# Kernel tuning notes

Hardware: AMD Instinct MI355X
Metric: run time of the kernel (lower is better)

The kernel has to match this reference:

```python
import jax, jax.numpy as jnp
import numpy as np

PH = 32          # prediction horizon (unroll steps)
HID = 512        # hidden_dim == latent_dim (output fed back as input)
OUT = 2          # output_dim
BS = 2048


def setup_inputs() -> dict:
    key = jax.random.key(0)
    ks = jax.random.split(key, 8)
    s = 1.0 / np.sqrt(HID)
    return {
        "hist": jax.random.normal(ks[0], (BS, 8, 2), dtype=jnp.float32),
        "z": jax.random.normal(ks[1], (BS, 1, HID), dtype=jnp.float32),
        # LSTMCell params (PyTorch layout: [4H, in], gate order i,f,g,o)
        "W_ih": jax.random.uniform(ks[2], (4 * HID, HID), jnp.float32, -s, s),
        "W_hh": jax.random.uniform(ks[3], (4 * HID, HID), jnp.float32, -s, s),
        "b_ih": jax.random.uniform(ks[4], (4 * HID,), jnp.float32, -s, s),
        "b_hh": jax.random.uniform(ks[5], (4 * HID,), jnp.float32, -s, s),
        # dense: hidden_dim -> output_dim
        "W_d": jax.random.uniform(ks[6], (OUT, HID), jnp.float32, -s, s),
        "b_d": jax.random.uniform(ks[7], (OUT,), jnp.float32, -s, s),
    }


def reference(hist, z, W_ih, W_hh, b_ih, b_hh, W_d, b_d):
    bs = z.shape[0]
    x0 = z.reshape(bs, -1)                       # [bs, H]
    h0 = jnp.zeros((bs, HID), dtype=z.dtype)
    c0 = jnp.zeros((bs, HID), dtype=z.dtype)

    def step(carry, _):
        x, h, c = carry
        gates = x @ W_ih.T + b_ih + h @ W_hh.T + b_hh   # [bs, 4H]
        i, f, g, o = jnp.split(gates, 4, axis=-1)
        c_new = jax.nn.sigmoid(f) * c + jax.nn.sigmoid(i) * jnp.tanh(g)
        h_new = jax.nn.sigmoid(o) * jnp.tanh(c_new)
        # output h is fed back as next input
        return (h_new, h_new, c_new), h_new

    _, hs = jax.lax.scan(step, (x0, h0, c0), None, length=PH)  # [PH, bs, H]
    out_all = jnp.swapaxes(hs, 0, 1)                           # [bs, PH, H]
    y = out_all @ W_d.T + b_d                                  # [bs, PH, OUT]
    return y
```

## Files before the change

kernel.cpp:

```cpp
#include <hip/hip_runtime.h>
#include <hip/hip_bf16.h>

#define BS_   2048
#define HID_  512
#define PH_   32

#define HWREG_XCC_ID ((3 << 11) | (0 << 6) | 20)

typedef _Float16 half8 __attribute__((ext_vector_type(8)));
typedef float floatx4 __attribute__((ext_vector_type(4)));

__device__ __forceinline__ float sigf(float x) { return 1.f / (1.f + __expf(-x)); }
__device__ __forceinline__ float tanhfast(float x) {
    float e = __expf(2.f * x);
    return 1.f - 2.f / (e + 1.f);
}

__global__ __launch_bounds__(256) void prep_kernel(
    const float* __restrict__ Wih, const float* __restrict__ Whh,
    const float* __restrict__ bih, const float* __restrict__ bhh,
    const float* __restrict__ z,
    _Float16* __restrict__ wih16, _Float16* __restrict__ wsum16,
    _Float16* __restrict__ z16, float* __restrict__ bsum,
    int* __restrict__ cnt)
{
    int i = blockIdx.x * 256 + threadIdx.x;
    if (i < BS_ * HID_) z16[i] = (_Float16)z[i];
    if (i < 4 * HID_ * HID_) {
        float a = Wih[i];
        wih16[i]  = (_Float16)a;
        wsum16[i] = (_Float16)(a + Whh[i]);
    }
    if (i < 4 * HID_) bsum[i] = bih[i] + bhh[i];
    if (i < 264) cnt[i] = 0;
}

__device__ __forceinline__ void stage_weights(_Float16* Wl, const _Float16* Wg,
                                              int j, int tid)
{
#pragma unroll
    for (int rep = 0; rep < 8; ++rep) {
        int idx = rep * 512 + tid;
        int n  = idx >> 6;
        int kb = idx & 63;
        int g  = n >> 4, u = n & 15;
        const half8* src = (const half8*)(Wg + ((size_t)(g * HID_ + j * 16 + u)) * HID_ + kb * 8);
        int phys = (kb & 56) | ((kb & 7) ^ (n & 7));
        *(half8*)((char*)Wl + n * 1024 + phys * 16) = *src;
    }
}

__global__ __launch_bounds__(512, 2) void lstm_persist(
    const _Float16* __restrict__ wih16, const _Float16* __restrict__ wsum16,
    const float* __restrict__ bsum, const _Float16* __restrict__ z16,
    _Float16* __restrict__ hs, int* __restrict__ cnt)
{
    __shared__ _Float16 Wl[64 * 512];

    const int tid  = threadIdx.x;
    const int ib   = blockIdx.x & 7;
    const int j    = blockIdx.x >> 3;
    const int lane = tid & 63;
    const int wv   = tid >> 6;
    const int qw   = lane >> 4;
    const int ln   = lane & 15;
    const int hid  = j * 16 + ln;

    stage_weights(Wl, wih16, j, tid);

    float bias[4];
#pragma unroll
    for (int g = 0; g < 4; ++g) bias[g] = bsum[g * HID_ + hid];

    float c[2][4];
#pragma unroll
    for (int mt = 0; mt < 2; ++mt)
#pragma unroll
        for (int r = 0; r < 4; ++r) c[mt][r] = 0.f;

    const char* Bl = (const char*)Wl;
    const int tE = (qw ^ (ln & 7)) * 16;

    bool fast = false;

    __syncthreads();

    for (int t = 0; t < PH_; ++t) {
        const _Float16* x = (t == 0) ? z16 : hs + (size_t)(t - 1) * BS_ * HID_;

        if (t >= 1) {
            if (tid == 0) {
                while (__hip_atomic_fetch_add(&cnt[ib * 32 + t - 1], 0,
                                              __ATOMIC_RELAXED,
                                              __HIP_MEMORY_SCOPE_AGENT) < 32) {
                    __builtin_amdgcn_s_sleep(1);
                }
                if (t == 1) {
                    __builtin_amdgcn_fence(__ATOMIC_ACQUIRE, "agent");
                    int m = __hip_atomic_fetch_add(&cnt[256 + ib], 0,
                                                   __ATOMIC_RELAXED,
                                                   __HIP_MEMORY_SCOPE_AGENT);
                    fast = (__popc((unsigned)m) == 1);
                } else if (fast) {
                    __builtin_amdgcn_fence(__ATOMIC_ACQUIRE, "workgroup");
                } else {
                    __builtin_amdgcn_fence(__ATOMIC_ACQUIRE, "agent");
                }
            }
            __syncthreads();
        }

        floatx4 acc[2][4];
#pragma unroll
        for (int mt = 0; mt < 2; ++mt)
#pragma unroll
            for (int g = 0; g < 4; ++g) acc[mt][g] = (floatx4){0.f, 0.f, 0.f, 0.f};

        const _Float16* A0 = x + (size_t)(ib * 256 + wv * 32 + ln) * HID_ + qw * 8;

#pragma unroll
        for (int kk = 0; kk < 16; ++kk) {
            half8 a0 = *(const half8*)(A0 + kk * 32);
            half8 a1 = *(const half8*)(A0 + 16 * HID_ + kk * 32);
            half8 b[4];
#pragma unroll
            for (int g = 0; g < 4; ++g) {
                int off = (g * 16 + ln) * 1024 + (kk >> 1) * 128 + (tE ^ ((kk & 1) << 6));
                b[g] = *(const half8*)(Bl + off);
            }
#pragma unroll
            for (int g = 0; g < 4; ++g) {
                acc[0][g] = __builtin_amdgcn_mfma_f32_16x16x32_f16(a0, b[g], acc[0][g], 0, 0, 0);
                acc[1][g] = __builtin_amdgcn_mfma_f32_16x16x32_f16(a1, b[g], acc[1][g], 0, 0, 0);
            }
        }

        _Float16* hb = hs + (size_t)t * BS_ * HID_
                          + (size_t)(ib * 256 + wv * 32 + qw * 4) * HID_ + hid;
#pragma unroll
        for (int mt = 0; mt < 2; ++mt) {
#pragma unroll
            for (int r = 0; r < 4; ++r) {
                float gi = acc[mt][0][r] + bias[0];
                float gf = acc[mt][1][r] + bias[1];
                float gg = acc[mt][2][r] + bias[2];
                float go = acc[mt][3][r] + bias[3];
                float cn = sigf(gf) * c[mt][r] + sigf(gi) * tanhfast(gg);
                float hn = sigf(go) * tanhfast(cn);
                c[mt][r] = cn;
                hb[(size_t)(mt * 16 + r) * HID_] = (_Float16)hn;
            }
        }

        __syncthreads();
        if (t == 0) {
            if (tid == 0) {
                int xcd = __builtin_amdgcn_s_getreg(HWREG_XCC_ID) & 0xf;
                __hip_atomic_fetch_or(&cnt[256 + ib], 1 << xcd,
                                      __ATOMIC_RELAXED, __HIP_MEMORY_SCOPE_AGENT);
                __threadfence();
                atomicAdd(&cnt[ib * 32 + 0], 1);
            }
            stage_weights(Wl, wsum16, j, tid);
            __syncthreads();
        } else if (t < PH_ - 1) {
            if (tid == 0) {
                if (fast) {
                    __hip_atomic_fetch_add(&cnt[ib * 32 + t], 1,
                                           __ATOMIC_RELAXED,
                                           __HIP_MEMORY_SCOPE_AGENT);
                } else {
                    __threadfence();
                    atomicAdd(&cnt[ib * 32 + t], 1);
                }
            }
        }
    }
}

__global__ __launch_bounds__(256) void dense_kernel(
    const _Float16* __restrict__ hs, const float* __restrict__ Wd,
    const float* __restrict__ bd, float* __restrict__ y)
{
    int gw   = (blockIdx.x * 256 + threadIdx.x) >> 6;
    int lane = threadIdx.x & 63;
    int tt = gw & 31, b = gw >> 5;
    half8 h = *(const half8*)(hs + ((size_t)tt * BS_ + b) * HID_ + lane * 8);
    float s0 = 0.f, s1 = 0.f;
#pragma unroll
    for (int k = 0; k < 8; ++k) {
        float hv = (float)h[k];
        s0 += hv * Wd[lane * 8 + k];
        s1 += hv * Wd[HID_ + lane * 8 + k];
    }
#pragma unroll
    for (int m = 32; m >= 1; m >>= 1) {
        s0 += __shfl_xor(s0, m);
        s1 += __shfl_xor(s1, m);
    }
    if (lane == 0) {
        float* o = y + ((size_t)b * PH_ + tt) * 2;
        o[0] = s0 + bd[0];
        o[1] = s1 + bd[1];
    }
}

extern "C" void kernel_launch(void* const* d_in, const int* in_sizes, int n_in,
                              void* d_out, int out_size, void* d_ws, size_t ws_size,
                              hipStream_t stream)
{
    (void)in_sizes; (void)n_in; (void)out_size; (void)ws_size;
    const float* z   = (const float*)d_in[1];
    const float* Wih = (const float*)d_in[2];
    const float* Whh = (const float*)d_in[3];
    const float* bih = (const float*)d_in[4];
    const float* bhh = (const float*)d_in[5];
    const float* Wd  = (const float*)d_in[6];
    const float* bd  = (const float*)d_in[7];
    float* y = (float*)d_out;

    char* ws = (char*)d_ws;
    _Float16* hs     = (_Float16*)ws;
    _Float16* z16    = (_Float16*)(ws + (size_t)67108864);
    _Float16* wih16  = (_Float16*)(ws + (size_t)69206016);
    _Float16* wsum16 = (_Float16*)(ws + (size_t)71303168);
    float*    bsum   = (float*)   (ws + (size_t)73400320);
    int*      cnt    = (int*)     (ws + (size_t)73408512);

    prep_kernel<<<4096, 256, 0, stream>>>(Wih, Whh, bih, bhh, z,
                                          wih16, wsum16, z16, bsum, cnt);

    {
        const void* k = (const void*)lstm_persist;
        void* args[] = {(void*)&wih16, (void*)&wsum16, (void*)&bsum,
                        (void*)&z16, (void*)&hs, (void*)&cnt};
        hipLaunchCooperativeKernel(k, dim3(256), dim3(512), args, 0, stream);
    }

    dense_kernel<<<16384, 256, 0, stream>>>(hs, Wd, bd, y);
}
```

Before: 474.1 us.

## Assign LSTM work tiles by XCD at runtime and software-pipeline MFMA operand loads

Each workgroup reads its XCC id and claims a slot so that all 32 column-blocks of one batch group land on the same XCD. Leftover workgroups take unclaimed slots after two grid barriers. This lets more groups use the cheaper workgroup-scope fence path for per-step synchronisation instead of agent-scope fences. The inner GEMM loop now prefetches A fragments four steps ahead and double-buffers the LDS B fragments, and the bias is folded into the accumulator initialisation. The cost is two extra grid barriers at startup and higher register pressure.

```diff
diff --git a/kernel.cpp b/kernel.cpp
--- a/kernel.cpp
+++ b/kernel.cpp
@@ -6,6 +6,14 @@
 #define PH_   32
 
 #define HWREG_XCC_ID ((3 << 11) | (0 << 6) | 20)
+
+#define C_STEP  0
+#define C_MASK  256
+#define C_SLOT  264
+#define C_SPILL 272
+#define C_GSYNC 288
+#define C_TAKEN 320
+#define C_TOTAL 576
 
 typedef _Float16 half8 __attribute__((ext_vector_type(8)));
 typedef float floatx4 __attribute__((ext_vector_type(4)));
@@ -32,7 +40,21 @@
         wsum16[i] = (_Float16)(a + Whh[i]);
     }
     if (i < 4 * HID_) bsum[i] = bih[i] + bhh[i];
-    if (i < 264) cnt[i] = 0;
+    if (i < C_TOTAL) cnt[i] = 0;
+}
+
+__device__ __forceinline__ void grid_sync(int* gc, int tid) {
+    __syncthreads();
+    if (tid == 0) {
+        __threadfence();
+        atomicAdd(gc, 1);
+        while (__hip_atomic_fetch_add(gc, 0, __ATOMIC_RELAXED,
+                                      __HIP_MEMORY_SCOPE_AGENT) < 256) {
+            __builtin_amdgcn_s_sleep(1);
+        }
+        __builtin_amdgcn_fence(__ATOMIC_ACQUIRE, "agent");
+    }
+    __syncthreads();
 }
 
 __device__ __forceinline__ void stage_weights(_Float16* Wl, const _Float16* Wg,
@@ -56,14 +78,53 @@
     _Float16* __restrict__ hs, int* __restrict__ cnt)
 {
     __shared__ _Float16 Wl[64 * 512];
+    __shared__ int sh_ctrl;
 
     const int tid  = threadIdx.x;
-    const int ib   = blockIdx.x & 7;
-    const int j    = blockIdx.x >> 3;
     const int lane = tid & 63;
     const int wv   = tid >> 6;
     const int qw   = lane >> 4;
     const int ln   = lane & 15;
+
+    int x = 0, mine = -1, rank = -1;
+    if (tid == 0) {
+        x = __builtin_amdgcn_s_getreg(HWREG_XCC_ID) & 7;
+        int s = __hip_atomic_fetch_add(&cnt[C_SLOT + x], 1, __ATOMIC_RELAXED,
+                                       __HIP_MEMORY_SCOPE_AGENT);
+        if (s < 32) {
+            mine = x * 32 + s;
+            cnt[C_TAKEN + mine] = 1;
+            __hip_atomic_fetch_or(&cnt[C_MASK + x], 1 << x, __ATOMIC_RELAXED,
+                                  __HIP_MEMORY_SCOPE_AGENT);
+        } else {
+            rank = __hip_atomic_fetch_add(&cnt[C_SPILL], 1, __ATOMIC_RELAXED,
+                                          __HIP_MEMORY_SCOPE_AGENT);
+        }
+    }
+    grid_sync(&cnt[C_GSYNC + 0], tid);
+    if (tid == 0 && mine < 0) {
+        int seen = 0;
+        for (int s = 0; s < 256; ++s) {
+            if (cnt[C_TAKEN + s] == 0) {
+                if (seen == rank) { mine = s; break; }
+                ++seen;
+            }
+        }
+        __hip_atomic_fetch_or(&cnt[C_MASK + (mine >> 5)], 1 << x,
+                              __ATOMIC_RELAXED, __HIP_MEMORY_SCOPE_AGENT);
+    }
+    grid_sync(&cnt[C_GSYNC + 1], tid);
+    if (tid == 0) {
+        int m = __hip_atomic_fetch_add(&cnt[C_MASK + (mine >> 5)], 0,
+                                       __ATOMIC_RELAXED, __HIP_MEMORY_SCOPE_AGENT);
+        int fastf = (__popc((unsigned)m) == 1) ? 1 : 0;
+        sh_ctrl = mine | (fastf << 16);
+    }
+    __syncthreads();
+    const int ctrl = sh_ctrl;
+    const int ib   = (ctrl & 0xffff) >> 5;
+    const int j    = ctrl & 31;
+    const bool fast = (ctrl >> 16) != 0;
     const int hid  = j * 16 + ln;
 
     stage_weights(Wl, wih16, j, tid);
@@ -81,57 +142,64 @@
     const char* Bl = (const char*)Wl;
     const int tE = (qw ^ (ln & 7)) * 16;
 
-    bool fast = false;
-
     __syncthreads();
 
     for (int t = 0; t < PH_; ++t) {
-        const _Float16* x = (t == 0) ? z16 : hs + (size_t)(t - 1) * BS_ * HID_;
+        const _Float16* xx = (t == 0) ? z16 : hs + (size_t)(t - 1) * BS_ * HID_;
 
         if (t >= 1) {
             if (tid == 0) {
-                while (__hip_atomic_fetch_add(&cnt[ib * 32 + t - 1], 0,
+                while (__hip_atomic_fetch_add(&cnt[C_STEP + ib * 32 + t - 1], 0,
                                               __ATOMIC_RELAXED,
                                               __HIP_MEMORY_SCOPE_AGENT) < 32) {
                     __builtin_amdgcn_s_sleep(1);
                 }
-                if (t == 1) {
-                    __builtin_amdgcn_fence(__ATOMIC_ACQUIRE, "agent");
-                    int m = __hip_atomic_fetch_add(&cnt[256 + ib], 0,
-                                                   __ATOMIC_RELAXED,
-                                                   __HIP_MEMORY_SCOPE_AGENT);
-                    fast = (__popc((unsigned)m) == 1);
-                } else if (fast) {
-                    __builtin_amdgcn_fence(__ATOMIC_ACQUIRE, "workgroup");
-                } else {
-                    __builtin_amdgcn_fence(__ATOMIC_ACQUIRE, "agent");
+                if (fast) __builtin_amdgcn_fence(__ATOMIC_ACQUIRE, "workgroup");
+                else      __builtin_amdgcn_fence(__ATOMIC_ACQUIRE, "agent");
+            }
+            __syncthreads();
+        }
+
+        floatx4 acc[2][4];
+#pragma unroll
+        for (int mt = 0; mt < 2; ++mt)
+#pragma unroll
+            for (int g = 0; g < 4; ++g)
+                acc[mt][g] = (floatx4){bias[g], bias[g], bias[g], bias[g]};
+
+        const _Float16* A0 = xx + (size_t)(ib * 256 + wv * 32 + ln) * HID_ + qw * 8;
+
+        half8 a0r[4], a1r[4], bA[4], bB[4];
+#pragma unroll
+        for (int p = 0; p < 4; ++p) {
+            a0r[p] = *(const half8*)(A0 + p * 32);
+            a1r[p] = *(const half8*)(A0 + 16 * HID_ + p * 32);
+        }
+#pragma unroll
+        for (int g = 0; g < 4; ++g)
+            bA[g] = *(const half8*)(Bl + (g * 16 + ln) * 1024 + tE);
+
+#pragma unroll
+        for (int kk = 0; kk < 16; ++kk) {
+            half8 ca0 = a0r[kk & 3], ca1 = a1r[kk & 3];
+            if (kk < 12) {
+                a0r[kk & 3] = *(const half8*)(A0 + (kk + 4) * 32);
+                a1r[kk & 3] = *(const half8*)(A0 + 16 * HID_ + (kk + 4) * 32);
+            }
+            half8* cb = (kk & 1) ? bB : bA;
+            half8* nb = (kk & 1) ? bA : bB;
+            if (kk < 15) {
+                int k1 = kk + 1;
+#pragma unroll
+                for (int g = 0; g < 4; ++g) {
+                    int off = (g * 16 + ln) * 1024 + (k1 >> 1) * 128 + (tE ^ ((k1 & 1) << 6));
+                    nb[g] = *(const half8*)(Bl + off);
                 }
             }
-            __syncthreads();
-        }
-
-        floatx4 acc[2][4];
-#pragma unroll
-        for (int mt = 0; mt < 2; ++mt)
-#pragma unroll
-            for (int g = 0; g < 4; ++g) acc[mt][g] = (floatx4){0.f, 0.f, 0.f, 0.f};
-
-        const _Float16* A0 = x + (size_t)(ib * 256 + wv * 32 + ln) * HID_ + qw * 8;
-
-#pragma unroll
-        for (int kk = 0; kk < 16; ++kk) {
-            half8 a0 = *(const half8*)(A0 + kk * 32);
-            half8 a1 = *(const half8*)(A0 + 16 * HID_ + kk * 32);
-            half8 b[4];
 #pragma unroll
             for (int g = 0; g < 4; ++g) {
-                int off = (g * 16 + ln) * 1024 + (kk >> 1) * 128 + (tE ^ ((kk & 1) << 6));
-                b[g] = *(const half8*)(Bl + off);
-            }
-#pragma unroll
-            for (int g = 0; g < 4; ++g) {
-                acc[0][g] = __builtin_amdgcn_mfma_f32_16x16x32_f16(a0, b[g], acc[0][g], 0, 0, 0);
-                acc[1][g] = __builtin_amdgcn_mfma_f32_16x16x32_f16(a1, b[g], acc[1][g], 0, 0, 0);
+                acc[0][g] = __builtin_amdgcn_mfma_f32_16x16x32_f16(ca0, cb[g], acc[0][g], 0, 0, 0);
+                acc[1][g] = __builtin_amdgcn_mfma_f32_16x16x32_f16(ca1, cb[g], acc[1][g], 0, 0, 0);
             }
         }
 
@@ -141,10 +209,10 @@
         for (int mt = 0; mt < 2; ++mt) {
 #pragma unroll
             for (int r = 0; r < 4; ++r) {
-                float gi = acc[mt][0][r] + bias[0];
-                float gf = acc[mt][1][r] + bias[1];
-                float gg = acc[mt][2][r] + bias[2];
-                float go = acc[mt][3][r] + bias[3];
+                float gi = acc[mt][0][r];
+                float gf = acc[mt][1][r];
+                float gg = acc[mt][2][r];
+                float go = acc[mt][3][r];
                 float cn = sigf(gf) * c[mt][r] + sigf(gi) * tanhfast(gg);
                 float hn = sigf(go) * tanhfast(cn);
                 c[mt][r] = cn;
@@ -155,23 +223,24 @@
         __syncthreads();
         if (t == 0) {
             if (tid == 0) {
-                int xcd = __builtin_amdgcn_s_getreg(HWREG_XCC_ID) & 0xf;
-                __hip_atomic_fetch_or(&cnt[256 + ib], 1 << xcd,
-                                      __ATOMIC_RELAXED, __HIP_MEMORY_SCOPE_AGENT);
-                __threadfence();
-                atomicAdd(&cnt[ib * 32 + 0], 1);
+                if (fast) {
+                    __hip_atomic_fetch_add(&cnt[C_STEP + ib * 32], 1,
+                                           __ATOMIC_RELAXED, __HIP_MEMORY_SCOPE_AGENT);
+                } else {
+                    __threadfence();
+                    atomicAdd(&cnt[C_STEP + ib * 32], 1);
+                }
             }
             stage_weights(Wl, wsum16, j, tid);
             __syncthreads();
         } else if (t < PH_ - 1) {
             if (tid == 0) {
                 if (fast) {
-                    __hip_atomic_fetch_add(&cnt[ib * 32 + t], 1,
-                                           __ATOMIC_RELAXED,
-                                           __HIP_MEMORY_SCOPE_AGENT);
+                    __hip_atomic_fetch_add(&cnt[C_STEP + ib * 32 + t], 1,
+                                           __ATOMIC_RELAXED, __HIP_MEMORY_SCOPE_AGENT);
                 } else {
                     __threadfence();
-                    atomicAdd(&cnt[ib * 32 + t], 1);
+                    atomicAdd(&cnt[C_STEP + ib * 32 + t], 1);
                 }
             }
         }
```

Measured after the change: 484.5 us. 1.02x slower.
